# Performance work log

Hardware: AMD Instinct MI355X
Metric: run time of the kernel (lower is better)

The kernel has to match this reference:

```python
import jax, jax.numpy as jnp
import numpy as np

B = 64      # graphs in data1 batch
K = 50      # SortAggregation k
NPG = 1600  # nodes per graph in data1 (equal-size, contiguous batch vector)


def gcn_layer(x, src, dst, ew, W, b):
    # PyG GCNConv with edge_weight: add self loops (weight 1), symmetric norm.
    n = x.shape[0]
    idx = jnp.arange(n)
    src2 = jnp.concatenate([src, idx])
    dst2 = jnp.concatenate([dst, idx])
    ew2 = jnp.concatenate([ew, jnp.ones((n,), x.dtype)])
    deg = jax.ops.segment_sum(ew2, dst2, num_segments=n)
    dinv = jnp.where(deg > 0, jax.lax.rsqrt(deg), 0.0)
    norm = dinv[src2] * ew2 * dinv[dst2]
    h = x @ W                                   # [n, out]
    out = jax.ops.segment_sum(h[src2] * norm[:, None], dst2, num_segments=n)
    return out + b


def gnn(x, ei, ew, Wg1, bg1, Wg2, bg2):
    src, dst = ei[0], ei[1]
    h = jax.nn.relu(gcn_layer(x, src, dst, ew, Wg1, bg1))
    return jax.nn.relu(gcn_layer(h, src, dst, ew, Wg2, bg2))


def layer_norm(x, g, b, eps=1e-5):
    m = jnp.mean(x, -1, keepdims=True)
    v = jnp.mean((x - m) ** 2, -1, keepdims=True)
    return (x - m) * jax.lax.rsqrt(v + eps) * g + b


def setup_inputs() -> dict:
    key = jax.random.key(0)
    ks = jax.random.split(key, 16)
    N1, N2, F, E1, E2 = B * NPG, 199, 128, 1638400, 3184
    s = 0.05
    inp = {}
    inp["x1"] = jax.random.normal(ks[0], (N1, F), jnp.float32)
    inp["edge_attr1"] = jax.random.uniform(ks[1], (E1,), jnp.float32)
    inp["x2"] = jax.random.normal(ks[2], (N2, F), jnp.float32)
    inp["edge_attr2"] = jax.random.uniform(ks[3], (E2,), jnp.float32)
    inp["Wg1"] = jax.random.normal(ks[4], (F, 128), jnp.float32) * s
    inp["bg1"] = jnp.zeros((128,), jnp.float32)
    inp["Wg2"] = jax.random.normal(ks[5], (128, 64), jnp.float32) * s
    inp["bg2"] = jnp.zeros((64,), jnp.float32)
    inp["fc1_W"] = jax.random.normal(ks[6], (K * N2, 128), jnp.float32) * s
    inp["fc1_b"] = jnp.zeros((128,), jnp.float32)
    inp["ln1_g"] = jnp.ones((128,), jnp.float32)
    inp["ln1_b"] = jnp.zeros((128,), jnp.float32)
    inp["fc2_W"] = jax.random.normal(ks[7], (128, 64), jnp.float32) * s
    inp["fc2_b"] = jnp.zeros((64,), jnp.float32)
    inp["ln2_g"] = jnp.ones((64,), jnp.float32)
    inp["ln2_b"] = jnp.zeros((64,), jnp.float32)
    inp["fc3_W"] = jax.random.normal(ks[8], (64, 1), jnp.float32) * s
    inp["fc3_b"] = jnp.zeros((1,), jnp.float32)
    inp["edge_index1"] = jax.random.randint(ks[9], (2, E1), 0, N1)
    inp["edge_index2"] = jax.random.randint(ks[10], (2, E2), 0, N2)
    inp["batch1"] = jnp.repeat(jnp.arange(B), NPG)
    return inp


def reference(x1, edge_attr1, x2, edge_attr2, Wg1, bg1, Wg2, bg2,
              fc1_W, fc1_b, ln1_g, ln1_b, fc2_W, fc2_b, ln2_g, ln2_b,
              fc3_W, fc3_b, edge_index1, edge_index2, batch1):
    o1 = gnn(x1, edge_index1, edge_attr1, Wg1, bg1, Wg2, bg2)   # [N1, 64]
    o2 = gnn(x2, edge_index2, edge_attr2, Wg1, bg1, Wg2, bg2)   # [N2, 64]
    # torch.cdist(p=2) via gram trick (stable sqrt)
    d2 = (jnp.sum(o1 * o1, 1)[:, None] + jnp.sum(o2 * o2, 1)[None, :]
          - 2.0 * (o1 @ o2.T))
    dist = jnp.sqrt(jnp.maximum(d2, 0.0) + 1e-12)               # [N1, N2]
    # SortAggregation: batch1 is contiguous with equal-size graphs -> reshape
    dense = dist.reshape(B, NPG, -1)                            # [B, NPG, N2]
    _, idx = jax.lax.top_k(dense[:, :, -1], K)   # sort desc by last channel
    pooled = jnp.take_along_axis(dense, idx[:, :, None], axis=1)  # [B, K, N2]
    h = pooled.reshape(B, -1) @ fc1_W + fc1_b                   # [B, 128]
    h = jax.nn.relu(layer_norm(h, ln1_g, ln1_b))
    h = jax.nn.relu(layer_norm(h @ fc2_W + fc2_b, ln2_g, ln2_b))
    return jax.nn.sigmoid(h @ fc3_W + fc3_b)                    # [B, 1]
```

## Files before the change

kernel.cpp:

```cpp
#include <hip/hip_runtime.h>
#include <hip/hip_bf16.h>
#include <cstdint>


__device__ __forceinline__ int rfl(int v) { return __builtin_amdgcn_readfirstlane(v); }

__device__ __forceinline__ unsigned short f2bf(float f) {
    unsigned u = __float_as_uint(f);
    u = (u + 0x7fffu + ((u >> 16) & 1u)) >> 16;
    return (unsigned short)u;
}
__device__ __forceinline__ float lo16(unsigned v) { return __uint_as_float(v << 16); }
__device__ __forceinline__ float hi16(unsigned v) { return __uint_as_float(v & 0xffff0000u); }

#define BSHIFT 7
#define BNODES 128
#define BCAP 3072

__global__ void bhist_kernel(const int* __restrict__ dst, int* bcnt, int E, int nbuk) {
    __shared__ int bins[832];
    int t = threadIdx.x;
    for (int i = t; i < nbuk; i += 256) bins[i] = 0;
    __syncthreads();
    for (int e = blockIdx.x * 256 + t; e < E; e += gridDim.x * 256)
        atomicAdd(&bins[dst[e] >> BSHIFT], 1);
    __syncthreads();
    for (int i = t; i < nbuk; i += 256) {
        int v = bins[i];
        if (v) atomicAdd(&bcnt[i], v);
    }
}

__global__ void bscan_kernel(const int* __restrict__ bcnt, int* __restrict__ boff,
                             int* __restrict__ bcur, int* __restrict__ off,
                             int nbuk, int E, int N1) {
    __shared__ int carry_s;
    int lane = threadIdx.x;
    if (lane == 0) carry_s = 0;
    __syncthreads();
    for (int base = 0; base < nbuk; base += 64) {
        int i = base + lane;
        int v = (i < nbuk) ? bcnt[i] : 0;
        int s = v;
        for (int d2 = 1; d2 < 64; d2 <<= 1) { int u = __shfl_up(s, d2); if (lane >= d2) s += u; }
        int c = carry_s;
        if (i < nbuk) { boff[i] = c + s - v; bcur[i] = c + s - v; }
        __syncthreads();
        if (lane == 63) carry_s = c + s;
        __syncthreads();
    }
    if (lane == 0) { boff[nbuk] = E; off[N1] = E; }
}

#define BP_EPB 16384
__global__ __launch_bounds__(1024) void bpart_kernel(const int* __restrict__ dst,
                                                     const int* __restrict__ src,
                                                     const float* __restrict__ ew,
                                                     int* bcur, int2* __restrict__ stag,
                                                     int E, int nbuk) {
    __shared__ int cnt[832];
    __shared__ int base[832];
    int t = threadIdx.x;
    int e0 = blockIdx.x * BP_EPB;
    for (int i = t; i < nbuk; i += 1024) cnt[i] = 0;
    __syncthreads();
#pragma unroll
    for (int k = 0; k < 16; k++) {
        int e = e0 + k * 1024 + t;
        if (e < E) atomicAdd(&cnt[dst[e] >> BSHIFT], 1);
    }
    __syncthreads();
    for (int i = t; i < nbuk; i += 1024) {
        int c = cnt[i];
        base[i] = c ? atomicAdd(&bcur[i], c) : 0;
    }
    __syncthreads();
    for (int i = t; i < nbuk; i += 1024) cnt[i] = 0;
    __syncthreads();
#pragma unroll
    for (int k = 0; k < 16; k++) {
        int e = e0 + k * 1024 + t;
        if (e < E) {
            int d = dst[e];
            int b = d >> BSHIFT, dl = d & (BNODES - 1);
            int l = atomicAdd(&cnt[b], 1);
            stag[base[b] + l] = make_int2((src[e] & 0xFFFFF) | (dl << 20),
                                          __float_as_int(ew[e]));
        }
    }
}

__global__ __launch_bounds__(256) void bfine_kernel(const int2* __restrict__ stag,
                                                    const int* __restrict__ boff,
                                                    int2* __restrict__ packed,
                                                    int* __restrict__ off,
                                                    float* __restrict__ dinv,
                                                    int nbuk, int N1) {
    __shared__ int2 ein[BCAP];
    __shared__ int2 eout[BCAP];
    __shared__ float ews[BNODES];
    __shared__ int hist[BNODES];
    __shared__ int sb[BNODES];
    __shared__ int cnt2[BNODES];
    int b = blockIdx.x, t = threadIdx.x;
    int base = boff[b], nE = boff[b + 1] - base;
    bool staged = (nE <= BCAP);
    if (t < BNODES) { hist[t] = 0; ews[t] = 0.f; cnt2[t] = 0; }
    __syncthreads();
    if (staged)
        for (int i = t; i < nE; i += 256) ein[i] = stag[base + i];
    __syncthreads();
    for (int i = t; i < nE; i += 256) {
        int2 m = staged ? ein[i] : stag[base + i];
        int dl = m.x >> 20;
        atomicAdd(&hist[dl], 1);
        atomicAdd(&ews[dl], __int_as_float(m.y));
    }
    __syncthreads();
    if (t < 64) {
        int v0 = hist[t]; int s0 = v0;
        for (int d2 = 1; d2 < 64; d2 <<= 1) { int u = __shfl_up(s0, d2); if (t >= d2) s0 += u; }
        sb[t] = s0 - v0;
        int tot0 = __shfl(s0, 63);
        int v1 = hist[64 + t]; int s1 = v1;
        for (int d2 = 1; d2 < 64; d2 <<= 1) { int u = __shfl_up(s1, d2); if (t >= d2) s1 += u; }
        sb[64 + t] = tot0 + s1 - v1;
    }
    __syncthreads();
    int node = b * BNODES + t;
    if (t < BNODES && node < N1) {
        off[node] = base + sb[t];
        dinv[node] = rsqrtf(1.0f + ews[t]);
    }
    __syncthreads();
    for (int i = t; i < nE; i += 256) {
        int2 m = staged ? ein[i] : stag[base + i];
        int dl = m.x >> 20;
        int l = atomicAdd(&cnt2[dl], 1);
        int2 o = make_int2(m.x & 0xFFFFF, m.y);
        if (staged) eout[sb[dl] + l] = o;
        else packed[base + sb[dl] + l] = o;
    }
    __syncthreads();
    if (staged)
        for (int i = t; i < nE; i += 256) packed[base + i] = eout[i];
}

__global__ __launch_bounds__(256) void gemm128_kernel(const float* __restrict__ x,
                                                      const float* __restrict__ w,
                                                      const float* __restrict__ dinv,
                                                      unsigned short* __restrict__ outb,
                                                      int nrows) {
    __shared__ float ws[64 * 128];
    __shared__ float xs[64 * 68];
    int t = threadIdx.x;
    size_t r0 = (size_t)blockIdx.x * 64;
    int tx = t % 16, ty = t / 16;
    float acc[4][8];
#pragma unroll
    for (int i = 0; i < 4; i++)
#pragma unroll
        for (int j = 0; j < 8; j++) acc[i][j] = 0.f;

    for (int half = 0; half < 2; half++) {
        __syncthreads();
        for (int f = t; f < 64 * 32; f += 256)
            ((float4*)ws)[f] = ((const float4*)(w + half * 64 * 128))[f];
        for (int f = t; f < 64 * 16; f += 256) {
            int row = f >> 4, c4 = f & 15;
            float4 v = *((const float4*)(x + (r0 + row) * 128 + half * 64 + c4 * 4));
            *((float4*)(xs + row * 68 + c4 * 4)) = v;
        }
        __syncthreads();
        for (int k = 0; k < 64; k++) {
            float4 b0 = *((const float4*)(ws + k * 128 + tx * 8));
            float4 b1 = *((const float4*)(ws + k * 128 + tx * 8 + 4));
            float bb[8] = {b0.x, b0.y, b0.z, b0.w, b1.x, b1.y, b1.z, b1.w};
#pragma unroll
            for (int i = 0; i < 4; i++) {
                float a = xs[(ty * 4 + i) * 68 + k];
#pragma unroll
                for (int j = 0; j < 8; j++) acc[i][j] = fmaf(a, bb[j], acc[i][j]);
            }
        }
    }
#pragma unroll
    for (int i = 0; i < 4; i++) {
        size_t row = r0 + ty * 4 + i;
        float dv = dinv[row];
        uint4 pk;
        pk.x = (unsigned)f2bf(acc[i][0] * dv) | ((unsigned)f2bf(acc[i][1] * dv) << 16);
        pk.y = (unsigned)f2bf(acc[i][2] * dv) | ((unsigned)f2bf(acc[i][3] * dv) << 16);
        pk.z = (unsigned)f2bf(acc[i][4] * dv) | ((unsigned)f2bf(acc[i][5] * dv) << 16);
        pk.w = (unsigned)f2bf(acc[i][6] * dv) | ((unsigned)f2bf(acc[i][7] * dv) << 16);
        *((uint4*)(outb + row * 128 + tx * 8)) = pk;
    }
}

__global__ __launch_bounds__(256) void gemm64b_kernel(const float* __restrict__ x,
                                                      const float* __restrict__ w,
                                                      const float* __restrict__ dinv,
                                                      unsigned short* __restrict__ outb,
                                                      int nrows) {
    __shared__ float ws[64 * 64];
    __shared__ float xs[64 * 68];
    int t = threadIdx.x;
    size_t r0 = (size_t)blockIdx.x * 64;
    int tx = t % 8, ty = t / 8;
    float acc[2][8];
#pragma unroll
    for (int i = 0; i < 2; i++)
#pragma unroll
        for (int j = 0; j < 8; j++) acc[i][j] = 0.f;

    for (int half = 0; half < 2; half++) {
        __syncthreads();
        for (int f = t; f < 64 * 16; f += 256)
            ((float4*)ws)[f] = ((const float4*)(w + half * 64 * 64))[f];
        for (int f = t; f < 64 * 16; f += 256) {
            int row = f >> 4, c4 = f & 15;
            float4 v = *((const float4*)(x + (r0 + row) * 128 + half * 64 + c4 * 4));
            *((float4*)(xs + row * 68 + c4 * 4)) = v;
        }
        __syncthreads();
        for (int k = 0; k < 64; k++) {
            float4 b0 = *((const float4*)(ws + k * 64 + tx * 8));
            float4 b1 = *((const float4*)(ws + k * 64 + tx * 8 + 4));
            float bb[8] = {b0.x, b0.y, b0.z, b0.w, b1.x, b1.y, b1.z, b1.w};
#pragma unroll
            for (int i = 0; i < 2; i++) {
                float a = xs[(ty * 2 + i) * 68 + k];
#pragma unroll
                for (int j = 0; j < 8; j++) acc[i][j] = fmaf(a, bb[j], acc[i][j]);
            }
        }
    }
#pragma unroll
    for (int i = 0; i < 2; i++) {
        size_t row = r0 + ty * 2 + i;
        float dv = dinv[row];
        uint2 pk;
        pk.x = (unsigned)f2bf(acc[i][0] * dv) | ((unsigned)f2bf(acc[i][1] * dv) << 16);
        pk.y = (unsigned)f2bf(acc[i][2] * dv) | ((unsigned)f2bf(acc[i][3] * dv) << 16);
        *((uint2*)(outb + row * 64 + tx * 8)) = pk;
        pk.x = (unsigned)f2bf(acc[i][4] * dv) | ((unsigned)f2bf(acc[i][5] * dv) << 16);
        pk.y = (unsigned)f2bf(acc[i][6] * dv) | ((unsigned)f2bf(acc[i][7] * dv) << 16);
        *((uint2*)(outb + row * 64 + tx * 8 + 4)) = pk;
    }
}

__global__ __launch_bounds__(256) void agg128_kernel(const unsigned short* __restrict__ zs,
                                                     const int2* __restrict__ packed,
                                                     const int* __restrict__ off,
                                                     const float* __restrict__ dinv,
                                                     const float* __restrict__ bias,
                                                     float* __restrict__ h, int n) {
    int wid = threadIdx.x >> 6;
    int lane = threadIdx.x & 63;
    int d = rfl(blockIdx.x * 4 + wid);
    if (d >= n) return;
    const unsigned short* zl = zs + lane * 2;
    float dv = dinv[d];
    unsigned sv = *((const unsigned*)(zl + (size_t)d * 128));
    float acc0 = lo16(sv), acc1 = hi16(sv);
    float2 bv = *((const float2*)(bias + lane * 2));
    int e0 = off[d], e1 = off[d + 1];
    int e = e0;
    for (; e + 4 <= e1; e += 4) {
        int2 m0 = packed[e], m1 = packed[e + 1], m2 = packed[e + 2], m3 = packed[e + 3];
        int s0 = rfl(m0.x), s1 = rfl(m1.x), s2i = rfl(m2.x), s3 = rfl(m3.x);
        float w0 = __int_as_float(rfl(m0.y)), w1 = __int_as_float(rfl(m1.y));
        float w2v = __int_as_float(rfl(m2.y)), w3 = __int_as_float(rfl(m3.y));
        unsigned v0 = *((const unsigned*)(zl + (size_t)s0 * 128));
        unsigned v1 = *((const unsigned*)(zl + (size_t)s1 * 128));
        unsigned v2 = *((const unsigned*)(zl + (size_t)s2i * 128));
        unsigned v3 = *((const unsigned*)(zl + (size_t)s3 * 128));
        acc0 = fmaf(w0, lo16(v0), acc0); acc1 = fmaf(w0, hi16(v0), acc1);
        acc0 = fmaf(w1, lo16(v1), acc0); acc1 = fmaf(w1, hi16(v1), acc1);
        acc0 = fmaf(w2v, lo16(v2), acc0); acc1 = fmaf(w2v, hi16(v2), acc1);
        acc0 = fmaf(w3, lo16(v3), acc0); acc1 = fmaf(w3, hi16(v3), acc1);
    }
    for (; e < e1; e++) {
        int2 m = packed[e];
        int s = rfl(m.x);
        float w = __int_as_float(rfl(m.y));
        unsigned v = *((const unsigned*)(zl + (size_t)s * 128));
        acc0 = fmaf(w, lo16(v), acc0);
        acc1 = fmaf(w, hi16(v), acc1);
    }
    float2 hv = {fmaxf(dv * acc0 + bv.x, 0.f), fmaxf(dv * acc1 + bv.y, 0.f)};
    *((float2*)(h + (size_t)d * 128 + lane * 2)) = hv;
}

__global__ __launch_bounds__(256) void agg64_kernel(const unsigned short* __restrict__ zs2,
                                                    const int2* __restrict__ packed,
                                                    const int* __restrict__ off,
                                                    const float* __restrict__ dinv,
                                                    const float* __restrict__ bias,
                                                    float* __restrict__ o1buf, int n,
                                                    const float* __restrict__ o2,
                                                    const float* __restrict__ s2,
                                                    float* __restrict__ dlast, int N2) {
    int wid = threadIdx.x >> 6;
    int lane = threadIdx.x & 63;
    int d = rfl(blockIdx.x * 4 + wid);
    if (d >= n) return;
    const unsigned short* zl = zs2 + lane;
    float dv = dinv[d];
    float acc0 = __uint_as_float((unsigned)zl[(size_t)d * 64] << 16);
    float b0 = bias[lane];
    int e0 = off[d], e1 = off[d + 1];
    int e = e0;
    for (; e + 4 <= e1; e += 4) {
        int2 m0 = packed[e], m1 = packed[e + 1], m2 = packed[e + 2], m3 = packed[e + 3];
        int s0 = rfl(m0.x), s1 = rfl(m1.x), s2i = rfl(m2.x), s3 = rfl(m3.x);
        float w0 = __int_as_float(rfl(m0.y)), w1 = __int_as_float(rfl(m1.y));
        float w2v = __int_as_float(rfl(m2.y)), w3 = __int_as_float(rfl(m3.y));
        float v0 = __uint_as_float((unsigned)zl[(size_t)s0 * 64] << 16);
        float v1 = __uint_as_float((unsigned)zl[(size_t)s1 * 64] << 16);
        float v2 = __uint_as_float((unsigned)zl[(size_t)s2i * 64] << 16);
        float v3 = __uint_as_float((unsigned)zl[(size_t)s3 * 64] << 16);
        acc0 = fmaf(w0, v0, acc0);
        acc0 = fmaf(w1, v1, acc0);
        acc0 = fmaf(w2v, v2, acc0);
        acc0 = fmaf(w3, v3, acc0);
    }
    for (; e < e1; e++) {
        int2 m = packed[e];
        int s = rfl(m.x);
        float w = __int_as_float(rfl(m.y));
        acc0 = fmaf(w, __uint_as_float((unsigned)zl[(size_t)s * 64] << 16), acc0);
    }
    float a = fmaxf(dv * acc0 + b0, 0.f);
    o1buf[(size_t)d * 64 + lane] = a;
    float bl = o2[(size_t)(N2 - 1) * 64 + lane];
    float aa = a * a, ab = a * bl;
    for (int dd = 32; dd >= 1; dd >>= 1) {
        aa += __shfl_xor(aa, dd);
        ab += __shfl_xor(ab, dd);
    }
    if (lane == 0) {
        float d2 = aa + s2[N2 - 1] - 2.f * ab;
        dlast[d] = sqrtf(fmaxf(d2, 0.f) + 1e-12f);
    }
}

__global__ void g2_prep(const int* __restrict__ ei2, const float* __restrict__ ew2,
                        float* dinv2, float* a2a, float* a2b, int E2, int N2) {
    __shared__ float degl[256];
    int t = threadIdx.x;
    degl[t] = 1.0f;
    __syncthreads();
    for (int e = t; e < E2; e += 256) atomicAdd(&degl[ei2[E2 + e]], ew2[e]);
    __syncthreads();
    if (t < N2) dinv2[t] = rsqrtf(degl[t]);
    for (int i = t; i < N2 * 128; i += 256) a2a[i] = 0.f;
    for (int i = t; i < N2 * 64; i += 256) a2b[i] = 0.f;
}

template <int NCOL>
__global__ void g2_gemm(const float* __restrict__ x, const float* __restrict__ w,
                        float* __restrict__ z, int N2) {
    __shared__ float xr[128];
    int row = blockIdx.x, t = threadIdx.x;
    for (int k = t; k < 128; k += NCOL) xr[k] = x[row * 128 + k];
    __syncthreads();
    float acc = 0.f;
    for (int k = 0; k < 128; k++) acc = fmaf(xr[k], w[k * NCOL + t], acc);
    z[row * NCOL + t] = acc;
}

template <int C>
__global__ void g2_scatter(const float* __restrict__ z, const int* __restrict__ ei2,
                           const float* __restrict__ ew2, const float* __restrict__ dinv2,
                           float* a2, int E2) {
    constexpr int CPL = C / 64;
    int wid = threadIdx.x >> 6, lane = threadIdx.x & 63;
    int e = blockIdx.x * 4 + wid;
    if (e >= E2) return;
    int s = ei2[e], d = ei2[E2 + e];
    float nm = dinv2[s] * ew2[e] * dinv2[d];
#pragma unroll
    for (int q = 0; q < CPL; q++) {
        int c = lane * CPL + q;
        atomicAdd(&a2[d * C + c], nm * z[s * C + c]);
    }
}

__global__ void g2_fin128(const float* __restrict__ a2, const float* __restrict__ z,
                          const float* __restrict__ dinv2, const float* __restrict__ bias,
                          float* __restrict__ out, int N2) {
    int i = blockIdx.x * 256 + threadIdx.x;
    if (i >= N2 * 128) return;
    int n = i / 128, c = i % 128;
    float dv = dinv2[n];
    out[i] = fmaxf(a2[i] + dv * dv * z[i] + bias[c], 0.f);
}

__global__ void g2_fin64s2(const float* __restrict__ a2, const float* __restrict__ z,
                           const float* __restrict__ dinv2, const float* __restrict__ bias,
                           float* __restrict__ out, float* __restrict__ s2, int N2) {
    int wid = threadIdx.x >> 6, lane = threadIdx.x & 63;
    int row = blockIdx.x * 4 + wid;
    if (row >= N2) return;
    int i = row * 64 + lane;
    float dv = dinv2[row];
    float v = fmaxf(a2[i] + dv * dv * z[i] + bias[lane], 0.f);
    out[i] = v;
    float ss = v * v;
    for (int d = 32; d >= 1; d >>= 1) ss += __shfl_xor(ss, d);
    if (lane == 0) s2[row] = ss;
}

__global__ __launch_bounds__(256) void topk_kernel(const float* __restrict__ dlast,
                                                   int* __restrict__ topidx,
                                                   int NPG, int K) {
    __shared__ unsigned long long keys[1600];
    __shared__ unsigned long long wmax[4];
    int g = blockIdx.x, t = threadIdx.x;
    int lane = t & 63, wid = t >> 6;
    for (int r = t; r < NPG; r += 256) {
        unsigned vb = __float_as_uint(dlast[(size_t)g * NPG + r]);
        keys[r] = ((unsigned long long)vb << 32) | (unsigned)(NPG - 1 - r);
    }
    __syncthreads();
    for (int it = 0; it < K; it++) {
        unsigned long long m = 0ull;
        for (int r = t; r < NPG; r += 256) { unsigned long long k = keys[r]; if (k > m) m = k; }
        for (int d = 32; d >= 1; d >>= 1) {
            unsigned long long u = __shfl_xor(m, d);
            if (u > m) m = u;
        }
        if (lane == 0) wmax[wid] = m;
        __syncthreads();
        if (t == 0) {
            unsigned long long mm = wmax[0];
            for (int w = 1; w < 4; w++) if (wmax[w] > mm) mm = wmax[w];
            int rbest = NPG - 1 - (int)(mm & 0xffffffffull);
            topidx[g * K + it] = rbest;
            keys[rbest] = 0ull;
        }
        __syncthreads();
    }
}

__global__ void pooled_kernel(const float* __restrict__ o1, const float* __restrict__ o2,
                              const float* __restrict__ s2, const int* __restrict__ topidx,
                              float* __restrict__ pooled, int NPG, int K, int N2) {
    __shared__ float o1s[64];
    __shared__ float s1sh;
    int g = blockIdx.x / K, kk = blockIdx.x % K;
    int t = threadIdx.x;
    int r = topidx[g * K + kk];
    size_t node = (size_t)g * NPG + r;
    if (t < 64) o1s[t] = o1[node * 64 + t];
    __syncthreads();
    if (t < 64) {
        float v = o1s[t]; float ss = v * v;
        for (int d = 32; d >= 1; d >>= 1) ss += __shfl_xor(ss, d);
        if (t == 0) s1sh = ss;
    }
    __syncthreads();
    if (t < N2) {
        float dot = 0.f;
#pragma unroll 8
        for (int k2 = 0; k2 < 64; k2++) dot = fmaf(o1s[k2], o2[t * 64 + k2], dot);
        float d2 = s1sh + s2[t] - 2.f * dot;
        pooled[(size_t)blockIdx.x * N2 + t] = sqrtf(fmaxf(d2, 0.f) + 1e-12f);
    }
}

#define FC1_CH 256
__global__ __launch_bounds__(256) void fc1_kernel(const float* __restrict__ pooled,
                                                  const float* __restrict__ fc1W,
                                                  float* __restrict__ h1p,
                                                  int PK, int NCHUNK, int B) {
    __shared__ float ps[FC1_CH];
    __shared__ float red[256];
    int b = blockIdx.x % B, ch = blockIdx.x / B;
    int r0 = ch * FC1_CH;
    int nr = min(FC1_CH, PK - r0);
    int t = threadIdx.x;
    for (int i = t; i < nr; i += 256) ps[i] = pooled[(size_t)b * PK + r0 + i];
    __syncthreads();
    int c = t & 127, half = t >> 7;
    int rb = half * (FC1_CH / 2);
    int re = min(rb + FC1_CH / 2, nr);
    float acc = 0.f;
    for (int r = rb; r < re; r++)
        acc = fmaf(ps[r], fc1W[(size_t)(r0 + r) * 128 + c], acc);
    red[t] = acc;
    __syncthreads();
    if (t < 128) h1p[((size_t)b * NCHUNK + ch) * 128 + t] = red[t] + red[t + 128];
}

__global__ __launch_bounds__(256) void head2_kernel(
    const float* __restrict__ h1p, int NCHUNK,
    const float* __restrict__ fc1b, const float* __restrict__ ln1g,
    const float* __restrict__ ln1b, const float* __restrict__ fc2W,
    const float* __restrict__ fc2b, const float* __restrict__ ln2g,
    const float* __restrict__ ln2b, const float* __restrict__ fc3W,
    const float* __restrict__ fc3b, float* __restrict__ out) {
    __shared__ float red[256];
    __shared__ float h1[128];
    __shared__ float h2[64];
    int b = blockIdx.x, t = threadIdx.x;
    if (t < 128) {
        float s = 0.f;
        for (int ch = 0; ch < NCHUNK; ch++)
            s += h1p[((size_t)b * NCHUNK + ch) * 128 + t];
        h1[t] = s + fc1b[t];
    }
    __syncthreads();
    red[t] = (t < 128) ? h1[t] : 0.f;
    __syncthreads();
    for (int s = 128; s >= 1; s >>= 1) { if (t < s) red[t] += red[t + s]; __syncthreads(); }
    float mean1 = red[0] / 128.f;
    __syncthreads();
    float dv1 = (t < 128) ? (h1[t] - mean1) : 0.f;
    red[t] = dv1 * dv1;
    __syncthreads();
    for (int s = 128; s >= 1; s >>= 1) { if (t < s) red[t] += red[t + s]; __syncthreads(); }
    float var1 = red[0] / 128.f;
    __syncthreads();
    if (t < 128) {
        float y = (h1[t] - mean1) * rsqrtf(var1 + 1e-5f) * ln1g[t] + ln1b[t];
        h1[t] = fmaxf(y, 0.f);
    }
    __syncthreads();
    if (t < 64) {
        float a2v = 0.f;
        for (int k2 = 0; k2 < 128; k2++) a2v = fmaf(h1[k2], fc2W[k2 * 64 + t], a2v);
        h2[t] = a2v + fc2b[t];
    }
    __syncthreads();
    red[t] = (t < 64) ? h2[t] : 0.f;
    __syncthreads();
    for (int s = 128; s >= 1; s >>= 1) { if (t < s) red[t] += red[t + s]; __syncthreads(); }
    float mean2 = red[0] / 64.f;
    __syncthreads();
    float dv2 = (t < 64) ? (h2[t] - mean2) : 0.f;
    red[t] = dv2 * dv2;
    __syncthreads();
    for (int s = 128; s >= 1; s >>= 1) { if (t < s) red[t] += red[t + s]; __syncthreads(); }
    float var2 = red[0] / 64.f;
    __syncthreads();
    if (t < 64)
        h2[t] = fmaxf((h2[t] - mean2) * rsqrtf(var2 + 1e-5f) * ln2g[t] + ln2b[t], 0.f);
    __syncthreads();
    red[t] = (t < 64) ? h2[t] * fc3W[t] : 0.f;
    __syncthreads();
    for (int s = 128; s >= 1; s >>= 1) { if (t < s) red[t] += red[t + s]; __syncthreads(); }
    if (t == 0) out[b] = 1.f / (1.f + expf(-(red[0] + fc3b[0])));
}

extern "C" void kernel_launch(void* const* d_in, const int* in_sizes, int n_in,
                              void* d_out, int out_size, void* d_ws, size_t ws_size,
                              hipStream_t stream) {
    const float* x1   = (const float*)d_in[0];
    const float* ew1  = (const float*)d_in[1];
    const float* x2   = (const float*)d_in[2];
    const float* ew2  = (const float*)d_in[3];
    const float* Wg1  = (const float*)d_in[4];
    const float* bg1  = (const float*)d_in[5];
    const float* Wg2  = (const float*)d_in[6];
    const float* bg2  = (const float*)d_in[7];
    const float* fc1W = (const float*)d_in[8];
    const float* fc1b = (const float*)d_in[9];
    const float* ln1g = (const float*)d_in[10];
    const float* ln1b = (const float*)d_in[11];
    const float* fc2W = (const float*)d_in[12];
    const float* fc2b = (const float*)d_in[13];
    const float* ln2g = (const float*)d_in[14];
    const float* ln2b = (const float*)d_in[15];
    const float* fc3W = (const float*)d_in[16];
    const float* fc3b = (const float*)d_in[17];
    const int* ei1    = (const int*)d_in[18];
    const int* ei2    = (const int*)d_in[19];
    float* out = (float*)d_out;

    const int N1 = in_sizes[0] / 128;
    const int E1 = in_sizes[1];
    const int N2 = in_sizes[2] / 128;
    const int E2 = in_sizes[3];
    const int B  = out_size;
    const int NPG = N1 / B;
    const int K  = (in_sizes[8] / 128) / N2;
    const int PK = K * N2;
    const int NCHUNK = (PK + FC1_CH - 1) / FC1_CH;
    const int NBUK = (N1 + BNODES - 1) / BNODES;

    char* wsb = (char*)d_ws;
    size_t o = 0;
    auto alloc = [&](size_t bytes) -> void* {
        void* p = wsb + o;
        o += (bytes + 255) & ~(size_t)255;
        return p;
    };
    int*   bcnt   = (int*)alloc((size_t)NBUK * 4);
    int*   boff   = (int*)alloc((size_t)(NBUK + 1) * 4);
    int*   bcur   = (int*)alloc((size_t)NBUK * 4);
    int2*  stag   = (int2*)alloc((size_t)E1 * 8);
    int2*  packed = (int2*)alloc((size_t)E1 * 8);
    int*   off    = (int*)alloc((size_t)(N1 + 1) * 4);
    float* dinv1  = (float*)alloc((size_t)N1 * 4);
    unsigned short* zs1 = (unsigned short*)alloc((size_t)N1 * 128 * 2);
    float* h      = (float*)alloc((size_t)N1 * 128 * 4);
    unsigned short* zs2 = (unsigned short*)alloc((size_t)N1 * 64 * 2);
    float* o1buf  = (float*)alloc((size_t)N1 * 64 * 4);
    float* dl     = (float*)alloc((size_t)N1 * 4);
    int*   tki    = (int*)alloc((size_t)B * K * 4);
    float* pooled = (float*)alloc((size_t)B * K * N2 * 4);
    float* h1p    = (float*)alloc((size_t)B * NCHUNK * 128 * 4);
    float* dinv2  = (float*)alloc((size_t)N2 * 4);
    float* z2g    = (float*)alloc((size_t)N2 * 128 * 4);
    float* h2b    = (float*)alloc((size_t)N2 * 128 * 4);
    float* a2a    = (float*)alloc((size_t)N2 * 128 * 4);
    float* zz2    = (float*)alloc((size_t)N2 * 64 * 4);
    float* a2b    = (float*)alloc((size_t)N2 * 64 * 4);
    float* o2b    = (float*)alloc((size_t)N2 * 64 * 4);
    float* s2     = (float*)alloc((size_t)N2 * 4);
    (void)ws_size; (void)n_in;

    const int* src1 = ei1;
    const int* dst1 = ei1 + E1;

    hipMemsetAsync(bcnt, 0, (size_t)NBUK * 4, stream);
    bhist_kernel<<<400, 256, 0, stream>>>(dst1, bcnt, E1, NBUK);
    bscan_kernel<<<1, 64, 0, stream>>>(bcnt, boff, bcur, off, NBUK, E1, N1);
    bpart_kernel<<<(E1 + BP_EPB - 1) / BP_EPB, 1024, 0, stream>>>(dst1, src1, ew1, bcur,
                                                                  stag, E1, NBUK);
    bfine_kernel<<<NBUK, 256, 0, stream>>>(stag, boff, packed, off, dinv1, NBUK, N1);

    gemm128_kernel<<<N1 / 64, 256, 0, stream>>>(x1, Wg1, dinv1, zs1, N1);
    agg128_kernel<<<N1 / 4, 256, 0, stream>>>(zs1, packed, off, dinv1, bg1, h, N1);
    gemm64b_kernel<<<N1 / 64, 256, 0, stream>>>(h, Wg2, dinv1, zs2, N1);

    g2_prep<<<1, 256, 0, stream>>>(ei2, ew2, dinv2, a2a, a2b, E2, N2);
    g2_gemm<128><<<N2, 128, 0, stream>>>(x2, Wg1, z2g, N2);
    g2_scatter<128><<<(E2 + 3) / 4, 256, 0, stream>>>(z2g, ei2, ew2, dinv2, a2a, E2);
    g2_fin128<<<(N2 * 128 + 255) / 256, 256, 0, stream>>>(a2a, z2g, dinv2, bg1, h2b, N2);
    g2_gemm<64><<<N2, 64, 0, stream>>>(h2b, Wg2, zz2, N2);
    g2_scatter<64><<<(E2 + 3) / 4, 256, 0, stream>>>(zz2, ei2, ew2, dinv2, a2b, E2);
    g2_fin64s2<<<(N2 + 3) / 4, 256, 0, stream>>>(a2b, zz2, dinv2, bg2, o2b, s2, N2);

    agg64_kernel<<<N1 / 4, 256, 0, stream>>>(zs2, packed, off, dinv1, bg2, o1buf, N1,
                                             o2b, s2, dl, N2);

    topk_kernel<<<B, 256, 0, stream>>>(dl, tki, NPG, K);
    pooled_kernel<<<B * K, 256, 0, stream>>>(o1buf, o2b, s2, tki, pooled, NPG, K, N2);
    fc1_kernel<<<NCHUNK * B, 256, 0, stream>>>(pooled, fc1W, h1p, PK, NCHUNK, B);
    head2_kernel<<<B, 256, 0, stream>>>(h1p, NCHUNK, fc1b, ln1g, ln1b, fc2W, fc2b,
                                        ln2g, ln2b, fc3W, fc3b, out);
}
```

Measured before the change: 470.7 us.

## Restructure fc1 to load weight chunk once into registers and reuse across batch

The fc1 kernel previously launched one block per (batch, chunk) pair, so every fc1 weight row was re-read from global memory once per graph (64 times). The new version launches one block per 32-row chunk, keeps that weight slice in registers and multiplies it against all 64 batch rows staged in shared memory. This removes the repeated weight traffic. In exchange it uses more registers per thread, produces many more partial sums (NCHUNK grows eightfold), and the head kernel must reduce over more chunks.

```diff
diff --git a/kernel.cpp b/kernel.cpp
--- a/kernel.cpp
+++ b/kernel.cpp
@@ -470,28 +470,33 @@
     }
 }
 
-#define FC1_CH 256
+#define FC1_CH 32
 __global__ __launch_bounds__(256) void fc1_kernel(const float* __restrict__ pooled,
                                                   const float* __restrict__ fc1W,
                                                   float* __restrict__ h1p,
                                                   int PK, int NCHUNK, int B) {
-    __shared__ float ps[FC1_CH];
-    __shared__ float red[256];
-    int b = blockIdx.x % B, ch = blockIdx.x / B;
+    __shared__ float ps[64][FC1_CH];
+    int ch = blockIdx.x;
     int r0 = ch * FC1_CH;
     int nr = min(FC1_CH, PK - r0);
     int t = threadIdx.x;
-    for (int i = t; i < nr; i += 256) ps[i] = pooled[(size_t)b * PK + r0 + i];
-    __syncthreads();
-    int c = t & 127, half = t >> 7;
-    int rb = half * (FC1_CH / 2);
-    int re = min(rb + FC1_CH / 2, nr);
-    float acc = 0.f;
-    for (int r = rb; r < re; r++)
-        acc = fmaf(ps[r], fc1W[(size_t)(r0 + r) * 128 + c], acc);
-    red[t] = acc;
-    __syncthreads();
-    if (t < 128) h1p[((size_t)b * NCHUNK + ch) * 128 + t] = red[t] + red[t + 128];
+    for (int f = t; f < 64 * FC1_CH; f += 256) {
+        int b = f / FC1_CH, r = f % FC1_CH;
+        ps[b][r] = (r < nr && b < B) ? pooled[(size_t)b * PK + r0 + r] : 0.f;
+    }
+    int c = t & 127, bh = t >> 7;
+    float wreg[FC1_CH];
+#pragma unroll
+    for (int r = 0; r < FC1_CH; r++)
+        wreg[r] = (r < nr) ? fc1W[(size_t)(r0 + r) * 128 + c] : 0.f;
+    __syncthreads();
+    for (int bb = 0; bb < 32; bb++) {
+        int b = bh * 32 + bb;
+        float acc = 0.f;
+#pragma unroll
+        for (int r = 0; r < FC1_CH; r++) acc = fmaf(ps[b][r], wreg[r], acc);
+        if (b < B) h1p[((size_t)b * NCHUNK + ch) * 128 + c] = acc;
+    }
 }
 
 __global__ __launch_bounds__(256) void head2_kernel(
@@ -649,7 +654,7 @@
 
     topk_kernel<<<B, 256, 0, stream>>>(dl, tki, NPG, K);
     pooled_kernel<<<B * K, 256, 0, stream>>>(o1buf, o2b, s2, tki, pooled, NPG, K, N2);
-    fc1_kernel<<<NCHUNK * B, 256, 0, stream>>>(pooled, fc1W, h1p, PK, NCHUNK, B);
+    fc1_kernel<<<NCHUNK, 256, 0, stream>>>(pooled, fc1W, h1p, PK, NCHUNK, B);
     head2_kernel<<<B, 256, 0, stream>>>(h1p, NCHUNK, fc1b, ln1g, ln1b, fc2W, fc2b,
                                         ln2g, ln2b, fc3W, fc3b, out);
 }
```

New measurement: 491.9 us. +4.5%, slower.
